# Kernel tuning notes

Measured on AMD Instinct MI355X. Metric: run time of the kernel, lower is better.

Reference implementation:

```python
import jax, jax.numpy as jnp
import numpy as np

B, S, D = 4, 2048, 128

def _phi(x, W, d):
    # original: phi(x) = (1/sqrt(M)) * exp(-0.5*||x||_2) * exp(W @ x), M = d
    proj = jnp.exp(jnp.einsum('...d,md->...m', x, W))          # [..., d]
    scale = jnp.exp(-0.5 * jnp.linalg.norm(x, axis=-1, keepdims=True))
    return (scale / jnp.sqrt(jnp.asarray(d, x.dtype))) * proj

def setup_inputs() -> dict:
    key = jax.random.key(0)
    k1, k2, k3, k4 = jax.random.split(key, 4)
    # scale 0.1 keeps exp(W @ x) well within fp32 range
    K = jax.random.normal(k1, (B, S, D), dtype=jnp.float32) * 0.1
    Q = jax.random.normal(k2, (B, S, D), dtype=jnp.float32) * 0.1
    V = jax.random.normal(k3, (B, S, D), dtype=jnp.float32) * 0.1
    W_phi = jax.random.normal(k4, (D, D), dtype=jnp.float32)
    sent_embed_slice = jnp.zeros((B, 1), dtype=jnp.float32)
    return {"K": K, "Q": Q, "V": V, "sent_embed_slice": sent_embed_slice,
            "max_seq_length": S, "qkv_size": D, "W_phi": W_phi}

def reference(K, Q, V, sent_embed_slice, max_seq_length, qkv_size, W_phi):
    d = qkv_size
    phiK = _phi(K, W_phi, d)   # [B, S, d]
    phiQ = _phi(Q, W_phi, d)   # [B, S, d]
    Bn = K.shape[0]

    def step(carry, inp):
        Mst, Nst = carry                       # [B, d, d], [B, d]
        pk, v, pq = inp                        # each [B, d]
        Mst = Mst + pk[:, :, None] * v[:, None, :]   # cumulative outer product
        Nst = Nst + pk                               # cumulative feature sum
        num = jnp.einsum('bd,bde->be', pq, Mst)      # phi(q) @ M
        r = jnp.einsum('bd,bd->b', pq, Nst)          # phi(q) . N
        out = num / (r + jnp.sign(r) * 1e-6)[:, None]
        return (Mst, Nst), out

    init = (jnp.zeros((Bn, d, d), K.dtype), jnp.zeros((Bn, d), K.dtype))
    xs = (jnp.swapaxes(phiK, 0, 1), jnp.swapaxes(V, 0, 1), jnp.swapaxes(phiQ, 0, 1))
    _, outs = jax.lax.scan(step, init, xs)    # outs: [S, B, d]
    return jnp.swapaxes(outs, 0, 1)           # [B, S, d]
```

## Files before the change

kernel.cpp:

```cpp
#include <hip/hip_runtime.h>

typedef float v4 __attribute__((ext_vector_type(4)));
typedef short s8v __attribute__((ext_vector_type(8)));
typedef float f4v __attribute__((ext_vector_type(4)));
typedef unsigned short u16;
typedef u16 us4 __attribute__((ext_vector_type(4)));
typedef u16 us8 __attribute__((ext_vector_type(8)));

#define OFF_PHIKB 0
#define OFF_PHIQB 524288
#define OFF_KVTB  1048576
#define OFF_PMB   3145728
#define OFF_N32   5242880
#define OFF_PN    5275648

__device__ inline u16 f2bf(float f) {
  union { float f; unsigned u; } v; v.f = f;
  unsigned r = v.u + 0x7fffu + ((v.u >> 16) & 1u);
  return (u16)(r >> 16);
}
__device__ inline float bf2f(u16 h) {
  union { unsigned u; float f; } v; v.u = ((unsigned)h) << 16; return v.f;
}

__global__ __launch_bounds__(256) void phikv_kernel(
    const float* __restrict__ K, const float* __restrict__ Q,
    const float* __restrict__ V, const float* __restrict__ W,
    u16* __restrict__ phiKb, u16* __restrict__ phiQb,
    u16* __restrict__ KVTb, float* __restrict__ N32) {
  __shared__ __align__(16) u16 smem[27136];
  __shared__ float srowsq[64];
  __shared__ float scl[64];
  u16* Xb = smem;
  u16* Wb = smem + 8704;
  u16* Pb = smem;
  u16* KdT = smem + 8704;
  u16* Vt = smem + 17920;

  const int tid = threadIdx.x;
  const bool isK = (blockIdx.y == 0);
  const float* X = isK ? K : Q;
  u16* outPhi = isK ? phiKb : phiQb;
  const int row0 = blockIdx.x * 64;
  const int wv = tid >> 6;
  const int lane = tid & 63;
  const int q = lane >> 4;
  const int ln = lane & 15;

#pragma unroll
  for (int k = 0; k < 8; k++) {
    int j = tid + k * 256;
    int r = j >> 5;
    int c4 = (j & 31) * 4;
    v4 x = *(const v4*)&X[(size_t)(row0 + r) * 128 + c4];
    us4 xb;
    float p = 0.f;
#pragma unroll
    for (int i = 0; i < 4; i++) { xb[i] = f2bf(x[i]); p += x[i] * x[i]; }
    *(us4*)&Xb[r * 136 + c4] = xb;
    p += __shfl_down(p, 16, 32);
    p += __shfl_down(p, 8, 32);
    p += __shfl_down(p, 4, 32);
    p += __shfl_down(p, 2, 32);
    p += __shfl_down(p, 1, 32);
    if ((tid & 31) == 0) srowsq[r] = p;
  }
#pragma unroll
  for (int k = 0; k < 16; k++) {
    int j = tid + k * 256;
    int r = j >> 5;
    int c4 = (j & 31) * 4;
    v4 w = *(const v4*)&W[(size_t)r * 128 + c4];
    us4 wb;
#pragma unroll
    for (int i = 0; i < 4; i++) wb[i] = f2bf(w[i]);
    *(us4*)&Wb[r * 136 + c4] = wb;
  }
  __syncthreads();
  if (tid < 64)
    scl[tid] = 0.08838834764831845f * __expf(-0.5f * sqrtf(srowsq[tid]));

  f4v acc[8];
#pragma unroll
  for (int ct = 0; ct < 8; ct++) acc[ct] = (f4v){0.f, 0.f, 0.f, 0.f};
#pragma unroll
  for (int ks = 0; ks < 4; ks++) {
    s8v a = *(const s8v*)&Xb[(wv * 16 + ln) * 136 + ks * 32 + q * 8];
#pragma unroll
    for (int ct = 0; ct < 8; ct++) {
      s8v bb = *(const s8v*)&Wb[(ct * 16 + ln) * 136 + ks * 32 + q * 8];
      acc[ct] = __builtin_amdgcn_mfma_f32_16x16x32_bf16(a, bb, acc[ct], 0, 0, 0);
    }
  }
  __syncthreads();

#pragma unroll
  for (int ct = 0; ct < 8; ct++) {
    us4 col;
#pragma unroll
    for (int r = 0; r < 4; r++) {
      int row = wv * 16 + q * 4 + r;
      u16 hv = f2bf(scl[row] * __expf(acc[ct][r]));
      Pb[row * 136 + ct * 16 + ln] = hv;
      col[r] = hv;
    }
    if (isK) *(us4*)&KdT[(ct * 16 + ln) * 72 + wv * 16 + q * 4] = col;
  }
  if (isK) {
#pragma unroll
    for (int k = 0; k < 8; k++) {
      int j = tid + k * 256;
      int s = j >> 5;
      int e4 = (j & 31) * 4;
      v4 vv = *(const v4*)&V[(size_t)(row0 + s) * 128 + e4];
#pragma unroll
      for (int i = 0; i < 4; i++) Vt[(e4 + i) * 72 + s] = f2bf(vv[i]);
    }
  }
  __syncthreads();

#pragma unroll
  for (int k = 0; k < 4; k++) {
    int j = tid + k * 256;
    int r = j >> 4;
    int d8 = (j & 15) * 8;
    *(us8*)&outPhi[(size_t)(row0 + r) * 128 + d8] = *(const us8*)&Pb[r * 136 + d8];
  }
  if (!isK) return;

  const int b = row0 >> 11;
  const int cgB = (row0 >> 5) & 63;

  {
    int c = tid >> 7;
    int d = tid & 127;
    float ns = 0.f;
#pragma unroll
    for (int s = 0; s < 32; s++) ns += bf2f(KdT[d * 72 + c * 32 + s]);
    N32[(size_t)(b * 64 + cgB + c) * 128 + d] = ns;
  }

#pragma unroll
  for (int c = 0; c < 2; c++) {
#pragma unroll
    for (int ei = 0; ei < 2; ei++) {
      const int et = wv * 2 + ei;
      s8v a = *(const s8v*)&Vt[(et * 16 + ln) * 72 + c * 32 + q * 8];
      f4v ac[8];
#pragma unroll
      for (int dt = 0; dt < 8; dt++) ac[dt] = (f4v){0.f, 0.f, 0.f, 0.f};
#pragma unroll
      for (int dt = 0; dt < 8; dt++) {
        s8v bb = *(const s8v*)&KdT[(dt * 16 + ln) * 72 + c * 32 + q * 8];
        ac[dt] = __builtin_amdgcn_mfma_f32_16x16x32_bf16(a, bb, ac[dt], 0, 0, 0);
      }
#pragma unroll
      for (int dt = 0; dt < 8; dt++)
#pragma unroll
        for (int r = 0; r < 4; r++) {
          int e = et * 16 + q * 4 + r;
          int d = dt * 16 + ln;
          KVTb[((size_t)(b * 128 + e) * 64 + (cgB + c)) * 128 + d] =
              f2bf(ac[dt][r]);
        }
    }
  }
}

__global__ __launch_bounds__(128) void prefix_kernel(
    const u16* __restrict__ KVTb, const float* __restrict__ N32,
    u16* __restrict__ PMb, float* __restrict__ PN) {
  const int tid = threadIdx.x;
  const int bid = blockIdx.x;
  if (bid < 512) {
    const size_t base = (size_t)bid * 64 * 128;
    float acc = 0.f;
#pragma unroll 8
    for (int c = 0; c < 64; c++) {
      PMb[base + c * 128 + tid] = f2bf(acc);
      acc += bf2f(KVTb[base + c * 128 + tid]);
    }
  } else {
    const int b = bid - 512;
    float acc = 0.f;
#pragma unroll 8
    for (int c = 0; c < 64; c++) {
      PN[(size_t)(b * 64 + c) * 128 + tid] = acc;
      acc += N32[(size_t)(b * 64 + c) * 128 + tid];
    }
  }
}

__global__ __launch_bounds__(256) void out_kernel(
    const u16* __restrict__ phiKb, const u16* __restrict__ phiQb,
    const float* __restrict__ V, const u16* __restrict__ PMb,
    const float* __restrict__ PN, float* __restrict__ out) {
  __shared__ __align__(16) u16 Qs[32][136];
  __shared__ __align__(16) u16 Ms[128][136];
  __shared__ __align__(16) u16 KsVt[128 * 40];
  __shared__ __align__(16) u16 Ps[32][40];
  __shared__ float Ns[128];
  __shared__ float rs[32];

  const int tid = threadIdx.x;
  const int b = blockIdx.x >> 6;
  const int c = blockIdx.x & 63;
  const int srow0 = b * 2048 + c * 32;
  const int wave = tid >> 6;
  const int lane = tid & 63;
  const int q = lane >> 4;
  const int ln = lane & 15;

#pragma unroll
  for (int k = 0; k < 2; k++) {
    int j = tid + k * 256;
    int t = j >> 4;
    int d8 = (j & 15) * 8;
    *(us8*)&Qs[t][d8] = *(const us8*)&phiQb[(size_t)(srow0 + t) * 128 + d8];
    *(us8*)&KsVt[t * 136 + d8] =
        *(const us8*)&phiKb[(size_t)(srow0 + t) * 128 + d8];
  }
#pragma unroll
  for (int k = 0; k < 8; k++) {
    int j = tid + k * 256;
    int e = j >> 4;
    int d8 = (j & 15) * 8;
    *(us8*)&Ms[e][d8] =
        *(const us8*)&PMb[((size_t)(b * 128 + e) * 64 + c) * 128 + d8];
  }
  if (tid < 128) Ns[tid] = PN[(size_t)(b * 64 + c) * 128 + tid];
  __syncthreads();

  {
    const int tr = wave >> 1, tc = wave & 1;
    f4v acc = {0.f, 0.f, 0.f, 0.f};
#pragma unroll
    for (int ks = 0; ks < 4; ks++) {
      s8v a = *(const s8v*)&Qs[tr * 16 + ln][ks * 32 + q * 8];
      s8v bb = *(const s8v*)&KsVt[(tc * 16 + ln) * 136 + ks * 32 + q * 8];
      acc = __builtin_amdgcn_mfma_f32_16x16x32_bf16(a, bb, acc, 0, 0, 0);
    }
    const int s_g = tc * 16 + ln;
#pragma unroll
    for (int r = 0; r < 4; r++) {
      int t_g = tr * 16 + q * 4 + r;
      Ps[t_g][s_g] = f2bf(s_g <= t_g ? acc[r] : 0.f);
    }
  }
  __syncthreads();

#pragma unroll
  for (int k = 0; k < 4; k++) {
    int j = tid + k * 256;
    int s = j & 31;
    int e4 = (j >> 5) * 4;
    v4 vv = *(const v4*)&V[(size_t)(srow0 + s) * 128 + e4];
#pragma unroll
    for (int i = 0; i < 4; i++) KsVt[(e4 + i) * 40 + s] = f2bf(vv[i]);
  }
  {
    const int t = tid >> 3;
    const int p8 = tid & 7;
    float rsl = 0.f;
#pragma unroll
    for (int s = p8; s < 32; s += 8) rsl += bf2f(Ps[t][s]);
#pragma unroll
    for (int d = p8; d < 128; d += 8) rsl += bf2f(Qs[t][d]) * Ns[d];
    rsl += __shfl_down(rsl, 4, 8);
    rsl += __shfl_down(rsl, 2, 8);
    rsl += __shfl_down(rsl, 1, 8);
    if (p8 == 0) rs[t] = rsl;
  }
  __syncthreads();

  const int e0 = wave * 32;
  f4v acc2[2][2];
#pragma unroll
  for (int i = 0; i < 2; i++)
#pragma unroll
    for (int j = 0; j < 2; j++) acc2[i][j] = (f4v){0.f, 0.f, 0.f, 0.f};

#pragma unroll
  for (int tr2 = 0; tr2 < 2; tr2++) {
    s8v a_p = *(const s8v*)&Ps[tr2 * 16 + ln][q * 8];
#pragma unroll
    for (int tc2 = 0; tc2 < 2; tc2++) {
      s8v b_v = *(const s8v*)&KsVt[(e0 + tc2 * 16 + ln) * 40 + q * 8];
      acc2[tr2][tc2] =
          __builtin_amdgcn_mfma_f32_16x16x32_bf16(a_p, b_v, acc2[tr2][tc2], 0, 0, 0);
    }
  }
#pragma unroll
  for (int ks = 0; ks < 4; ks++) {
#pragma unroll
    for (int tr2 = 0; tr2 < 2; tr2++) {
      s8v a_q = *(const s8v*)&Qs[tr2 * 16 + ln][ks * 32 + q * 8];
#pragma unroll
      for (int tc2 = 0; tc2 < 2; tc2++) {
        s8v b_m = *(const s8v*)&Ms[e0 + tc2 * 16 + ln][ks * 32 + q * 8];
        acc2[tr2][tc2] =
            __builtin_amdgcn_mfma_f32_16x16x32_bf16(a_q, b_m, acc2[tr2][tc2], 0, 0, 0);
      }
    }
  }

#pragma unroll
  for (int tr2 = 0; tr2 < 2; tr2++) {
#pragma unroll
    for (int r = 0; r < 4; r++) {
      int t_g = tr2 * 16 + q * 4 + r;
      float rv = rs[t_g];
      float den = rv + (rv > 0.f ? 1e-6f : (rv < 0.f ? -1e-6f : 0.f));
      float inv = 1.f / den;
#pragma unroll
      for (int tc2 = 0; tc2 < 2; tc2++) {
        int e_g = e0 + tc2 * 16 + ln;
        out[(size_t)(srow0 + t_g) * 128 + e_g] = acc2[tr2][tc2][r] * inv;
      }
    }
  }
}

extern "C" void kernel_launch(void* const* d_in, const int* in_sizes, int n_in,
                              void* d_out, int out_size, void* d_ws,
                              size_t ws_size, hipStream_t stream) {
  (void)in_sizes; (void)n_in; (void)out_size; (void)ws_size;
  const float* K = (const float*)d_in[0];
  const float* Q = (const float*)d_in[1];
  const float* V = (const float*)d_in[2];
  const float* W = (const float*)d_in[6];
  float* out = (float*)d_out;
  float* ws = (float*)d_ws;

  u16* phiKb = (u16*)(ws + OFF_PHIKB);
  u16* phiQb = (u16*)(ws + OFF_PHIQB);
  u16* KVTb = (u16*)(ws + OFF_KVTB);
  u16* PMb = (u16*)(ws + OFF_PMB);
  float* N32 = ws + OFF_N32;
  float* PN = ws + OFF_PN;

  phikv_kernel<<<dim3(128, 2), 256, 0, stream>>>(K, Q, V, W, phiKb, phiQb,
                                                 KVTb, N32);
  prefix_kernel<<<516, 128, 0, stream>>>(KVTb, N32, PMb, PN);
  out_kernel<<<256, 256, 0, stream>>>(phiKb, phiQb, V, PMb, PN, out);
}
```

Measured before the change: 95.58 us.

## Fuse three kernels into one persistent kernel with grid-wide barriers

Merges the phi/KV, prefix-scan and output kernels into a single 256-block launch separated by atomic-counter grid barriers, and adds a memset to reset the counters before launch. This removes two kernel launch gaps. The prefix scan now runs on only 33 blocks using 8-wide vector loads, and V loads are issued early into registers to overlap with other work. The risks are that the scan is concentrated on few blocks while the rest wait at the barrier, and that the barrier relies on all 256 blocks being resident at once.

```diff
diff --git a/kernel.cpp b/kernel.cpp
--- a/kernel.cpp
+++ b/kernel.cpp
@@ -1,6 +1,7 @@
 #include <hip/hip_runtime.h>
 
 typedef float v4 __attribute__((ext_vector_type(4)));
+typedef float v2 __attribute__((ext_vector_type(2)));
 typedef short s8v __attribute__((ext_vector_type(8)));
 typedef float f4v __attribute__((ext_vector_type(4)));
 typedef unsigned short u16;
@@ -13,6 +14,7 @@
 #define OFF_PMB   3145728
 #define OFF_N32   5242880
 #define OFF_PN    5275648
+#define OFF_BAR   5308416
 
 __device__ inline u16 f2bf(float f) {
   union { float f; unsigned u; } v; v.f = f;
@@ -23,299 +25,341 @@
   union { unsigned u; float f; } v; v.u = ((unsigned)h) << 16; return v.f;
 }
 
-__global__ __launch_bounds__(256) void phikv_kernel(
+__device__ inline void grid_barrier(unsigned* ctr, unsigned target) {
+  __syncthreads();
+  if (threadIdx.x == 0) {
+    __threadfence();
+    __hip_atomic_fetch_add(ctr, 1u, __ATOMIC_RELEASE, __HIP_MEMORY_SCOPE_AGENT);
+    while (__hip_atomic_load(ctr, __ATOMIC_ACQUIRE, __HIP_MEMORY_SCOPE_AGENT) <
+           target) {
+      __builtin_amdgcn_s_sleep(8);
+    }
+    __threadfence();
+  }
+  __syncthreads();
+}
+
+__global__ __launch_bounds__(256) void fused_kernel(
     const float* __restrict__ K, const float* __restrict__ Q,
     const float* __restrict__ V, const float* __restrict__ W,
-    u16* __restrict__ phiKb, u16* __restrict__ phiQb,
-    u16* __restrict__ KVTb, float* __restrict__ N32) {
-  __shared__ __align__(16) u16 smem[27136];
-  __shared__ float srowsq[64];
-  __shared__ float scl[64];
-  u16* Xb = smem;
-  u16* Wb = smem + 8704;
-  u16* Pb = smem;
-  u16* KdT = smem + 8704;
-  u16* Vt = smem + 17920;
+    u16* __restrict__ phiKb, u16* __restrict__ phiQb, u16* __restrict__ KVTb,
+    float* __restrict__ N32, u16* __restrict__ PMb, float* __restrict__ PN,
+    float* __restrict__ out, unsigned* __restrict__ bar) {
+  __shared__ __align__(16) u16 smem[28160];
+  __shared__ float sfl[160];
 
   const int tid = threadIdx.x;
-  const bool isK = (blockIdx.y == 0);
-  const float* X = isK ? K : Q;
-  u16* outPhi = isK ? phiKb : phiQb;
-  const int row0 = blockIdx.x * 64;
+  const int bid = blockIdx.x;
   const int wv = tid >> 6;
   const int lane = tid & 63;
   const int q = lane >> 4;
   const int ln = lane & 15;
 
-#pragma unroll
-  for (int k = 0; k < 8; k++) {
-    int j = tid + k * 256;
-    int r = j >> 5;
-    int c4 = (j & 31) * 4;
-    v4 x = *(const v4*)&X[(size_t)(row0 + r) * 128 + c4];
-    us4 xb;
-    float p = 0.f;
-#pragma unroll
-    for (int i = 0; i < 4; i++) { xb[i] = f2bf(x[i]); p += x[i] * x[i]; }
-    *(us4*)&Xb[r * 136 + c4] = xb;
-    p += __shfl_down(p, 16, 32);
-    p += __shfl_down(p, 8, 32);
-    p += __shfl_down(p, 4, 32);
-    p += __shfl_down(p, 2, 32);
-    p += __shfl_down(p, 1, 32);
-    if ((tid & 31) == 0) srowsq[r] = p;
+  {
+    const bool isK = (bid & 1) == 0;
+    const int slab = bid >> 1;
+    const float* X = isK ? K : Q;
+    u16* outPhi = isK ? phiKb : phiQb;
+    const int row0 = slab * 64;
+    u16* Xb = smem;
+    u16* Wb = smem + 8704;
+    u16* Pb = smem;
+    u16* KdT = smem + 8704;
+    u16* Vt = smem + 17920;
+    float* srowsq = sfl;
+    float* scl = sfl + 64;
+
+    v4 vpre[8];
+    if (isK) {
+#pragma unroll
+      for (int k = 0; k < 8; k++) {
+        int j = tid + k * 256;
+        int s = j >> 5;
+        int e4 = (j & 31) * 4;
+        vpre[k] = *(const v4*)&V[(size_t)(row0 + s) * 128 + e4];
+      }
+    }
+
+#pragma unroll
+    for (int k = 0; k < 8; k++) {
+      int j = tid + k * 256;
+      int r = j >> 5;
+      int c4 = (j & 31) * 4;
+      v4 x = *(const v4*)&X[(size_t)(row0 + r) * 128 + c4];
+      us4 xb;
+      float p = 0.f;
+#pragma unroll
+      for (int i = 0; i < 4; i++) { xb[i] = f2bf(x[i]); p += x[i] * x[i]; }
+      *(us4*)&Xb[r * 136 + c4] = xb;
+      p += __shfl_down(p, 16, 32);
+      p += __shfl_down(p, 8, 32);
+      p += __shfl_down(p, 4, 32);
+      p += __shfl_down(p, 2, 32);
+      p += __shfl_down(p, 1, 32);
+      if ((tid & 31) == 0) srowsq[r] = p;
+    }
+#pragma unroll
+    for (int k = 0; k < 16; k++) {
+      int j = tid + k * 256;
+      int r = j >> 5;
+      int c4 = (j & 31) * 4;
+      v4 w = *(const v4*)&W[(size_t)r * 128 + c4];
+      us4 wb;
+#pragma unroll
+      for (int i = 0; i < 4; i++) wb[i] = f2bf(w[i]);
+      *(us4*)&Wb[r * 136 + c4] = wb;
+    }
+    __syncthreads();
+    if (tid < 64)
+      scl[tid] = 0.08838834764831845f * __expf(-0.5f * sqrtf(srowsq[tid]));
+
+    f4v acc[8];
+#pragma unroll
+    for (int ct = 0; ct < 8; ct++) acc[ct] = (f4v){0.f, 0.f, 0.f, 0.f};
+#pragma unroll
+    for (int ks = 0; ks < 4; ks++) {
+      s8v a = *(const s8v*)&Xb[(wv * 16 + ln) * 136 + ks * 32 + q * 8];
+#pragma unroll
+      for (int ct = 0; ct < 8; ct++) {
+        s8v bb = *(const s8v*)&Wb[(ct * 16 + ln) * 136 + ks * 32 + q * 8];
+        acc[ct] =
+            __builtin_amdgcn_mfma_f32_16x16x32_bf16(a, bb, acc[ct], 0, 0, 0);
+      }
+    }
+    __syncthreads();
+
+#pragma unroll
+    for (int ct = 0; ct < 8; ct++) {
+      us4 col;
+#pragma unroll
+      for (int r = 0; r < 4; r++) {
+        int row = wv * 16 + q * 4 + r;
+        u16 hv = f2bf(scl[row] * __expf(acc[ct][r]));
+        Pb[row * 136 + ct * 16 + ln] = hv;
+        col[r] = hv;
+      }
+      if (isK) *(us4*)&KdT[(ct * 16 + ln) * 72 + wv * 16 + q * 4] = col;
+    }
+    if (isK) {
+#pragma unroll
+      for (int k = 0; k < 8; k++) {
+        int j = tid + k * 256;
+        int s = j >> 5;
+        int e4 = (j & 31) * 4;
+#pragma unroll
+        for (int i = 0; i < 4; i++) Vt[(e4 + i) * 72 + s] = f2bf(vpre[k][i]);
+      }
+    }
+    __syncthreads();
+
+#pragma unroll
+    for (int k = 0; k < 4; k++) {
+      int j = tid + k * 256;
+      int r = j >> 4;
+      int d8 = (j & 15) * 8;
+      *(us8*)&outPhi[(size_t)(row0 + r) * 128 + d8] =
+          *(const us8*)&Pb[r * 136 + d8];
+    }
+    if (isK) {
+      const int b = row0 >> 11;
+      const int cgB = (row0 >> 5) & 63;
+      {
+        int c = tid >> 7;
+        int d = tid & 127;
+        float ns = 0.f;
+#pragma unroll
+        for (int s = 0; s < 32; s++) ns += bf2f(KdT[d * 72 + c * 32 + s]);
+        N32[(size_t)(b * 64 + cgB + c) * 128 + d] = ns;
+      }
+#pragma unroll
+      for (int c = 0; c < 2; c++) {
+#pragma unroll
+        for (int ei = 0; ei < 2; ei++) {
+          const int et = wv * 2 + ei;
+          s8v a = *(const s8v*)&Vt[(et * 16 + ln) * 72 + c * 32 + q * 8];
+          f4v ac[8];
+#pragma unroll
+          for (int dt = 0; dt < 8; dt++) ac[dt] = (f4v){0.f, 0.f, 0.f, 0.f};
+#pragma unroll
+          for (int dt = 0; dt < 8; dt++) {
+            s8v bb = *(const s8v*)&KdT[(dt * 16 + ln) * 72 + c * 32 + q * 8];
+            ac[dt] =
+                __builtin_amdgcn_mfma_f32_16x16x32_bf16(a, bb, ac[dt], 0, 0, 0);
+          }
+#pragma unroll
+          for (int dt = 0; dt < 8; dt++)
+#pragma unroll
+            for (int r = 0; r < 4; r++) {
+              int e = et * 16 + q * 4 + r;
+              int d = dt * 16 + ln;
+              KVTb[((size_t)(b * 128 + e) * 64 + (cgB + c)) * 128 + d] =
+                  f2bf(ac[dt][r]);
+            }
+        }
+      }
+    }
   }
-#pragma unroll
-  for (int k = 0; k < 16; k++) {
-    int j = tid + k * 256;
-    int r = j >> 5;
-    int c4 = (j & 31) * 4;
-    v4 w = *(const v4*)&W[(size_t)r * 128 + c4];
-    us4 wb;
-#pragma unroll
-    for (int i = 0; i < 4; i++) wb[i] = f2bf(w[i]);
-    *(us4*)&Wb[r * 136 + c4] = wb;
+  grid_barrier(bar + 0, 256);
+
+  if (bid < 32) {
+    const int r = bid * 16 + (tid >> 4);
+    const int d8 = (tid & 15) * 8;
+    const size_t base = (size_t)r * (64 * 128);
+    float acc[8];
+#pragma unroll
+    for (int i = 0; i < 8; i++) acc[i] = 0.f;
+#pragma unroll 4
+    for (int c = 0; c < 64; c++) {
+      us8 st;
+#pragma unroll
+      for (int i = 0; i < 8; i++) st[i] = f2bf(acc[i]);
+      *(us8*)&PMb[base + c * 128 + d8] = st;
+      us8 kv = *(const us8*)&KVTb[base + c * 128 + d8];
+#pragma unroll
+      for (int i = 0; i < 8; i++) acc[i] += bf2f(kv[i]);
+    }
+  } else if (bid == 32) {
+    const int b = tid >> 6;
+    const int d2 = (tid & 63) * 2;
+    float a0 = 0.f, a1 = 0.f;
+#pragma unroll 4
+    for (int c = 0; c < 64; c++) {
+      size_t idx = (size_t)(b * 64 + c) * 128 + d2;
+      *(v2*)&PN[idx] = (v2){a0, a1};
+      v2 nv = *(const v2*)&N32[idx];
+      a0 += nv[0];
+      a1 += nv[1];
+    }
   }
-  __syncthreads();
-  if (tid < 64)
-    scl[tid] = 0.08838834764831845f * __expf(-0.5f * sqrtf(srowsq[tid]));
-
-  f4v acc[8];
-#pragma unroll
-  for (int ct = 0; ct < 8; ct++) acc[ct] = (f4v){0.f, 0.f, 0.f, 0.f};
-#pragma unroll
-  for (int ks = 0; ks < 4; ks++) {
-    s8v a = *(const s8v*)&Xb[(wv * 16 + ln) * 136 + ks * 32 + q * 8];
-#pragma unroll
-    for (int ct = 0; ct < 8; ct++) {
-      s8v bb = *(const s8v*)&Wb[(ct * 16 + ln) * 136 + ks * 32 + q * 8];
-      acc[ct] = __builtin_amdgcn_mfma_f32_16x16x32_bf16(a, bb, acc[ct], 0, 0, 0);
-    }
-  }
-  __syncthreads();
-
-#pragma unroll
-  for (int ct = 0; ct < 8; ct++) {
-    us4 col;
-#pragma unroll
-    for (int r = 0; r < 4; r++) {
-      int row = wv * 16 + q * 4 + r;
-      u16 hv = f2bf(scl[row] * __expf(acc[ct][r]));
-      Pb[row * 136 + ct * 16 + ln] = hv;
-      col[r] = hv;
-    }
-    if (isK) *(us4*)&KdT[(ct * 16 + ln) * 72 + wv * 16 + q * 4] = col;
-  }
-  if (isK) {
+  grid_barrier(bar + 1, 256);
+
+  {
+    const int b = bid >> 6;
+    const int c = bid & 63;
+    const int srow0 = b * 2048 + c * 32;
+    u16* Qs = smem;
+    u16* Ms = smem + 4352;
+    u16* KsVt = smem + 21760;
+    u16* Ps = smem + 26880;
+    float* Ns = sfl;
+    float* rs = sfl + 128;
+
+    v4 vpre3[4];
+#pragma unroll
+    for (int k = 0; k < 4; k++) {
+      int j = tid + k * 256;
+      int s = j & 31;
+      int e4 = (j >> 5) * 4;
+      vpre3[k] = *(const v4*)&V[(size_t)(srow0 + s) * 128 + e4];
+    }
+
+#pragma unroll
+    for (int k = 0; k < 2; k++) {
+      int j = tid + k * 256;
+      int t = j >> 4;
+      int d8 = (j & 15) * 8;
+      *(us8*)&Qs[t * 136 + d8] =
+          *(const us8*)&phiQb[(size_t)(srow0 + t) * 128 + d8];
+      *(us8*)&KsVt[t * 136 + d8] =
+          *(const us8*)&phiKb[(size_t)(srow0 + t) * 128 + d8];
+    }
 #pragma unroll
     for (int k = 0; k < 8; k++) {
       int j = tid + k * 256;
-      int s = j >> 5;
-      int e4 = (j & 31) * 4;
-      v4 vv = *(const v4*)&V[(size_t)(row0 + s) * 128 + e4];
-#pragma unroll
-      for (int i = 0; i < 4; i++) Vt[(e4 + i) * 72 + s] = f2bf(vv[i]);
-    }
-  }
-  __syncthreads();
-
-#pragma unroll
-  for (int k = 0; k < 4; k++) {
-    int j = tid + k * 256;
-    int r = j >> 4;
-    int d8 = (j & 15) * 8;
-    *(us8*)&outPhi[(size_t)(row0 + r) * 128 + d8] = *(const us8*)&Pb[r * 136 + d8];
-  }
-  if (!isK) return;
-
-  const int b = row0 >> 11;
-  const int cgB = (row0 >> 5) & 63;
-
-  {
-    int c = tid >> 7;
-    int d = tid & 127;
-    float ns = 0.f;
-#pragma unroll
-    for (int s = 0; s < 32; s++) ns += bf2f(KdT[d * 72 + c * 32 + s]);
-    N32[(size_t)(b * 64 + cgB + c) * 128 + d] = ns;
-  }
-
-#pragma unroll
-  for (int c = 0; c < 2; c++) {
-#pragma unroll
-    for (int ei = 0; ei < 2; ei++) {
-      const int et = wv * 2 + ei;
-      s8v a = *(const s8v*)&Vt[(et * 16 + ln) * 72 + c * 32 + q * 8];
-      f4v ac[8];
-#pragma unroll
-      for (int dt = 0; dt < 8; dt++) ac[dt] = (f4v){0.f, 0.f, 0.f, 0.f};
-#pragma unroll
-      for (int dt = 0; dt < 8; dt++) {
-        s8v bb = *(const s8v*)&KdT[(dt * 16 + ln) * 72 + c * 32 + q * 8];
-        ac[dt] = __builtin_amdgcn_mfma_f32_16x16x32_bf16(a, bb, ac[dt], 0, 0, 0);
-      }
-#pragma unroll
-      for (int dt = 0; dt < 8; dt++)
-#pragma unroll
-        for (int r = 0; r < 4; r++) {
-          int e = et * 16 + q * 4 + r;
-          int d = dt * 16 + ln;
-          KVTb[((size_t)(b * 128 + e) * 64 + (cgB + c)) * 128 + d] =
-              f2bf(ac[dt][r]);
+      int e = j >> 4;
+      int d8 = (j & 15) * 8;
+      *(us8*)&Ms[e * 136 + d8] =
+          *(const us8*)&PMb[((size_t)(b * 128 + e) * 64 + c) * 128 + d8];
+    }
+    if (tid < 128) Ns[tid] = PN[(size_t)(b * 64 + c) * 128 + tid];
+    __syncthreads();
+
+    {
+      const int tr = wv >> 1, tc = wv & 1;
+      f4v acc = {0.f, 0.f, 0.f, 0.f};
+#pragma unroll
+      for (int ks = 0; ks < 4; ks++) {
+        s8v a = *(const s8v*)&Qs[(tr * 16 + ln) * 136 + ks * 32 + q * 8];
+        s8v bb = *(const s8v*)&KsVt[(tc * 16 + ln) * 136 + ks * 32 + q * 8];
+        acc = __builtin_amdgcn_mfma_f32_16x16x32_bf16(a, bb, acc, 0, 0, 0);
+      }
+      const int s_g = tc * 16 + ln;
+#pragma unroll
+      for (int r = 0; r < 4; r++) {
+        int t_g = tr * 16 + q * 4 + r;
+        Ps[t_g * 40 + s_g] = f2bf(s_g <= t_g ? acc[r] : 0.f);
+      }
+    }
+    __syncthreads();
+
+#pragma unroll
+    for (int k = 0; k < 4; k++) {
+      int j = tid + k * 256;
+      int s = j & 31;
+      int e4 = (j >> 5) * 4;
+#pragma unroll
+      for (int i = 0; i < 4; i++) KsVt[(e4 + i) * 40 + s] = f2bf(vpre3[k][i]);
+    }
+    {
+      const int t = tid >> 3;
+      const int p8 = tid & 7;
+      float rsl = 0.f;
+#pragma unroll
+      for (int s = p8; s < 32; s += 8) rsl += bf2f(Ps[t * 40 + s]);
+#pragma unroll
+      for (int d = p8; d < 128; d += 8) rsl += bf2f(Qs[t * 136 + d]) * Ns[d];
+      rsl += __shfl_down(rsl, 4, 8);
+      rsl += __shfl_down(rsl, 2, 8);
+      rsl += __shfl_down(rsl, 1, 8);
+      if (p8 == 0) rs[t] = rsl;
+    }
+    __syncthreads();
+
+    const int e0 = wv * 32;
+    f4v acc2[2][2];
+#pragma unroll
+    for (int i = 0; i < 2; i++)
+#pragma unroll
+      for (int j = 0; j < 2; j++) acc2[i][j] = (f4v){0.f, 0.f, 0.f, 0.f};
+
+#pragma unroll
+    for (int tr2 = 0; tr2 < 2; tr2++) {
+      s8v a_p = *(const s8v*)&Ps[(tr2 * 16 + ln) * 40 + q * 8];
+#pragma unroll
+      for (int tc2 = 0; tc2 < 2; tc2++) {
+        s8v b_v = *(const s8v*)&KsVt[(e0 + tc2 * 16 + ln) * 40 + q * 8];
+        acc2[tr2][tc2] = __builtin_amdgcn_mfma_f32_16x16x32_bf16(
+            a_p, b_v, acc2[tr2][tc2], 0, 0, 0);
+      }
+    }
+#pragma unroll
+    for (int ks = 0; ks < 4; ks++) {
+#pragma unroll
+      for (int tr2 = 0; tr2 < 2; tr2++) {
+        s8v a_q = *(const s8v*)&Qs[(tr2 * 16 + ln) * 136 + ks * 32 + q * 8];
+#pragma unroll
+        for (int tc2 = 0; tc2 < 2; tc2++) {
+          s8v b_m =
+              *(const s8v*)&Ms[(e0 + tc2 * 16 + ln) * 136 + ks * 32 + q * 8];
+          acc2[tr2][tc2] = __builtin_amdgcn_mfma_f32_16x16x32_bf16(
+              a_q, b_m, acc2[tr2][tc2], 0, 0, 0);
         }
-    }
-  }
-}
-
-__global__ __launch_bounds__(128) void prefix_kernel(
-    const u16* __restrict__ KVTb, const float* __restrict__ N32,
-    u16* __restrict__ PMb, float* __restrict__ PN) {
-  const int tid = threadIdx.x;
-  const int bid = blockIdx.x;
-  if (bid < 512) {
-    const size_t base = (size_t)bid * 64 * 128;
-    float acc = 0.f;
-#pragma unroll 8
-    for (int c = 0; c < 64; c++) {
-      PMb[base + c * 128 + tid] = f2bf(acc);
-      acc += bf2f(KVTb[base + c * 128 + tid]);
-    }
-  } else {
-    const int b = bid - 512;
-    float acc = 0.f;
-#pragma unroll 8
-    for (int c = 0; c < 64; c++) {
-      PN[(size_t)(b * 64 + c) * 128 + tid] = acc;
-      acc += N32[(size_t)(b * 64 + c) * 128 + tid];
-    }
-  }
-}
-
-__global__ __launch_bounds__(256) void out_kernel(
-    const u16* __restrict__ phiKb, const u16* __restrict__ phiQb,
-    const float* __restrict__ V, const u16* __restrict__ PMb,
-    const float* __restrict__ PN, float* __restrict__ out) {
-  __shared__ __align__(16) u16 Qs[32][136];
-  __shared__ __align__(16) u16 Ms[128][136];
-  __shared__ __align__(16) u16 KsVt[128 * 40];
-  __shared__ __align__(16) u16 Ps[32][40];
-  __shared__ float Ns[128];
-  __shared__ float rs[32];
-
-  const int tid = threadIdx.x;
-  const int b = blockIdx.x >> 6;
-  const int c = blockIdx.x & 63;
-  const int srow0 = b * 2048 + c * 32;
-  const int wave = tid >> 6;
-  const int lane = tid & 63;
-  const int q = lane >> 4;
-  const int ln = lane & 15;
-
-#pragma unroll
-  for (int k = 0; k < 2; k++) {
-    int j = tid + k * 256;
-    int t = j >> 4;
-    int d8 = (j & 15) * 8;
-    *(us8*)&Qs[t][d8] = *(const us8*)&phiQb[(size_t)(srow0 + t) * 128 + d8];
-    *(us8*)&KsVt[t * 136 + d8] =
-        *(const us8*)&phiKb[(size_t)(srow0 + t) * 128 + d8];
-  }
-#pragma unroll
-  for (int k = 0; k < 8; k++) {
-    int j = tid + k * 256;
-    int e = j >> 4;
-    int d8 = (j & 15) * 8;
-    *(us8*)&Ms[e][d8] =
-        *(const us8*)&PMb[((size_t)(b * 128 + e) * 64 + c) * 128 + d8];
-  }
-  if (tid < 128) Ns[tid] = PN[(size_t)(b * 64 + c) * 128 + tid];
-  __syncthreads();
-
-  {
-    const int tr = wave >> 1, tc = wave & 1;
-    f4v acc = {0.f, 0.f, 0.f, 0.f};
-#pragma unroll
-    for (int ks = 0; ks < 4; ks++) {
-      s8v a = *(const s8v*)&Qs[tr * 16 + ln][ks * 32 + q * 8];
-      s8v bb = *(const s8v*)&KsVt[(tc * 16 + ln) * 136 + ks * 32 + q * 8];
-      acc = __builtin_amdgcn_mfma_f32_16x16x32_bf16(a, bb, acc, 0, 0, 0);
-    }
-    const int s_g = tc * 16 + ln;
-#pragma unroll
-    for (int r = 0; r < 4; r++) {
-      int t_g = tr * 16 + q * 4 + r;
-      Ps[t_g][s_g] = f2bf(s_g <= t_g ? acc[r] : 0.f);
-    }
-  }
-  __syncthreads();
-
-#pragma unroll
-  for (int k = 0; k < 4; k++) {
-    int j = tid + k * 256;
-    int s = j & 31;
-    int e4 = (j >> 5) * 4;
-    v4 vv = *(const v4*)&V[(size_t)(srow0 + s) * 128 + e4];
-#pragma unroll
-    for (int i = 0; i < 4; i++) KsVt[(e4 + i) * 40 + s] = f2bf(vv[i]);
-  }
-  {
-    const int t = tid >> 3;
-    const int p8 = tid & 7;
-    float rsl = 0.f;
-#pragma unroll
-    for (int s = p8; s < 32; s += 8) rsl += bf2f(Ps[t][s]);
-#pragma unroll
-    for (int d = p8; d < 128; d += 8) rsl += bf2f(Qs[t][d]) * Ns[d];
-    rsl += __shfl_down(rsl, 4, 8);
-    rsl += __shfl_down(rsl, 2, 8);
-    rsl += __shfl_down(rsl, 1, 8);
-    if (p8 == 0) rs[t] = rsl;
-  }
-  __syncthreads();
-
-  const int e0 = wave * 32;
-  f4v acc2[2][2];
-#pragma unroll
-  for (int i = 0; i < 2; i++)
-#pragma unroll
-    for (int j = 0; j < 2; j++) acc2[i][j] = (f4v){0.f, 0.f, 0.f, 0.f};
-
-#pragma unroll
-  for (int tr2 = 0; tr2 < 2; tr2++) {
-    s8v a_p = *(const s8v*)&Ps[tr2 * 16 + ln][q * 8];
-#pragma unroll
-    for (int tc2 = 0; tc2 < 2; tc2++) {
-      s8v b_v = *(const s8v*)&KsVt[(e0 + tc2 * 16 + ln) * 40 + q * 8];
-      acc2[tr2][tc2] =
-          __builtin_amdgcn_mfma_f32_16x16x32_bf16(a_p, b_v, acc2[tr2][tc2], 0, 0, 0);
-    }
-  }
-#pragma unroll
-  for (int ks = 0; ks < 4; ks++) {
+      }
+    }
+
 #pragma unroll
     for (int tr2 = 0; tr2 < 2; tr2++) {
-      s8v a_q = *(const s8v*)&Qs[tr2 * 16 + ln][ks * 32 + q * 8];
-#pragma unroll
-      for (int tc2 = 0; tc2 < 2; tc2++) {
-        s8v b_m = *(const s8v*)&Ms[e0 + tc2 * 16 + ln][ks * 32 + q * 8];
-        acc2[tr2][tc2] =
-            __builtin_amdgcn_mfma_f32_16x16x32_bf16(a_q, b_m, acc2[tr2][tc2], 0, 0, 0);
-      }
-    }
-  }
-
-#pragma unroll
-  for (int tr2 = 0; tr2 < 2; tr2++) {
-#pragma unroll
-    for (int r = 0; r < 4; r++) {
-      int t_g = tr2 * 16 + q * 4 + r;
-      float rv = rs[t_g];
-      float den = rv + (rv > 0.f ? 1e-6f : (rv < 0.f ? -1e-6f : 0.f));
-      float inv = 1.f / den;
-#pragma unroll
-      for (int tc2 = 0; tc2 < 2; tc2++) {
-        int e_g = e0 + tc2 * 16 + ln;
-        out[(size_t)(srow0 + t_g) * 128 + e_g] = acc2[tr2][tc2][r] * inv;
+#pragma unroll
+      for (int r = 0; r < 4; r++) {
+        int t_g = tr2 * 16 + q * 4 + r;
+        float rv = rs[t_g];
+        float den = rv + (rv > 0.f ? 1e-6f : (rv < 0.f ? -1e-6f : 0.f));
+        float inv = 1.f / den;
+#pragma unroll
+        for (int tc2 = 0; tc2 < 2; tc2++) {
+          int e_g = e0 + tc2 * 16 + ln;
+          out[(size_t)(srow0 + t_g) * 128 + e_g] = acc2[tr2][tc2][r] * inv;
+        }
       }
     }
   }
@@ -338,9 +382,9 @@
   u16* PMb = (u16*)(ws + OFF_PMB);
   float* N32 = ws + OFF_N32;
   float* PN = ws + OFF_PN;
-
-  phikv_kernel<<<dim3(128, 2), 256, 0, stream>>>(K, Q, V, W, phiKb, phiQb,
-                                                 KVTb, N32);
-  prefix_kernel<<<516, 128, 0, stream>>>(KVTb, N32, PMb, PN);
-  out_kernel<<<256, 256, 0, stream>>>(phiKb, phiQb, V, PMb, PN, out);
-}
+  unsigned* bar = (unsigned*)(ws + OFF_BAR);
+
+  hipMemsetAsync(bar, 0, 2 * sizeof(unsigned), stream);
+  fused_kernel<<<256, 256, 0, stream>>>(K, Q, V, W, phiKb, phiQb, KVTb, N32,
+                                        PMb, PN, out, bar);
+}
```

Measured after the change: 180.6 us. 89.0% more time.

## Double chunk size to 64, split output by column quarters, vectorize prefix scan

Applied to the files above, without the earlier changes.

The sequence chunk size goes from 32 to 64. This halves the per-chunk KV state written to and read from the workspace, and halves the number of sequential prefix steps. phikv_kernel now runs 512 threads and issues its V loads early so they overlap the feature computation. The prefix kernel moves to 65 blocks with vectorized bf16 and float2 accesses. out_kernel splits each 64-row chunk into four 32-column slices, giving 512 blocks, and skips the masked upper-triangle MFMA tiles. The cost is that each slice block reloads the phiQ and phiK tiles and recomputes the intra-chunk score matrix and row sums.

```diff
diff --git a/kernel.cpp b/kernel.cpp
--- a/kernel.cpp
+++ b/kernel.cpp
@@ -1,18 +1,20 @@
 #include <hip/hip_runtime.h>
 
 typedef float v4 __attribute__((ext_vector_type(4)));
+typedef float v2 __attribute__((ext_vector_type(2)));
 typedef short s8v __attribute__((ext_vector_type(8)));
 typedef float f4v __attribute__((ext_vector_type(4)));
 typedef unsigned short u16;
+typedef u16 us2 __attribute__((ext_vector_type(2)));
 typedef u16 us4 __attribute__((ext_vector_type(4)));
 typedef u16 us8 __attribute__((ext_vector_type(8)));
 
 #define OFF_PHIKB 0
 #define OFF_PHIQB 524288
 #define OFF_KVTB  1048576
-#define OFF_PMB   3145728
-#define OFF_N32   5242880
-#define OFF_PN    5275648
+#define OFF_PMB   2097152
+#define OFF_N32   3145728
+#define OFF_PN    3162112
 
 __device__ inline u16 f2bf(float f) {
   union { float f; unsigned u; } v; v.f = f;
@@ -23,7 +25,7 @@
   union { unsigned u; float f; } v; v.u = ((unsigned)h) << 16; return v.f;
 }
 
-__global__ __launch_bounds__(256) void phikv_kernel(
+__global__ __launch_bounds__(512) void phikv_kernel(
     const float* __restrict__ K, const float* __restrict__ Q,
     const float* __restrict__ V, const float* __restrict__ W,
     u16* __restrict__ phiKb, u16* __restrict__ phiQb,
@@ -47,9 +49,21 @@
   const int q = lane >> 4;
   const int ln = lane & 15;
 
-#pragma unroll
-  for (int k = 0; k < 8; k++) {
-    int j = tid + k * 256;
+  v4 vpa[2], vpb[2];
+  if (isK) {
+#pragma unroll
+    for (int k = 0; k < 2; k++) {
+      int j = tid + k * 512;
+      int s0 = (j & 31) * 2;
+      int e4 = (j >> 5) * 4;
+      vpa[k] = *(const v4*)&V[(size_t)(row0 + s0) * 128 + e4];
+      vpb[k] = *(const v4*)&V[(size_t)(row0 + s0 + 1) * 128 + e4];
+    }
+  }
+
+#pragma unroll
+  for (int k = 0; k < 4; k++) {
+    int j = tid + k * 512;
     int r = j >> 5;
     int c4 = (j & 31) * 4;
     v4 x = *(const v4*)&X[(size_t)(row0 + r) * 128 + c4];
@@ -66,8 +80,8 @@
     if ((tid & 31) == 0) srowsq[r] = p;
   }
 #pragma unroll
-  for (int k = 0; k < 16; k++) {
-    int j = tid + k * 256;
+  for (int k = 0; k < 8; k++) {
+    int j = tid + k * 512;
     int r = j >> 5;
     int c4 = (j & 31) * 4;
     v4 w = *(const v4*)&W[(size_t)r * 128 + c4];
@@ -80,48 +94,53 @@
   if (tid < 64)
     scl[tid] = 0.08838834764831845f * __expf(-0.5f * sqrtf(srowsq[tid]));
 
-  f4v acc[8];
-#pragma unroll
-  for (int ct = 0; ct < 8; ct++) acc[ct] = (f4v){0.f, 0.f, 0.f, 0.f};
+  const int tr = wv >> 1;
+  const int cb = (wv & 1) * 4;
+  f4v acc[4];
+#pragma unroll
+  for (int i = 0; i < 4; i++) acc[i] = (f4v){0.f, 0.f, 0.f, 0.f};
 #pragma unroll
   for (int ks = 0; ks < 4; ks++) {
-    s8v a = *(const s8v*)&Xb[(wv * 16 + ln) * 136 + ks * 32 + q * 8];
-#pragma unroll
-    for (int ct = 0; ct < 8; ct++) {
-      s8v bb = *(const s8v*)&Wb[(ct * 16 + ln) * 136 + ks * 32 + q * 8];
-      acc[ct] = __builtin_amdgcn_mfma_f32_16x16x32_bf16(a, bb, acc[ct], 0, 0, 0);
-    }
-  }
-  __syncthreads();
-
-#pragma unroll
-  for (int ct = 0; ct < 8; ct++) {
+    s8v a = *(const s8v*)&Xb[(tr * 16 + ln) * 136 + ks * 32 + q * 8];
+#pragma unroll
+    for (int i = 0; i < 4; i++) {
+      s8v bb = *(const s8v*)&Wb[((cb + i) * 16 + ln) * 136 + ks * 32 + q * 8];
+      acc[i] = __builtin_amdgcn_mfma_f32_16x16x32_bf16(a, bb, acc[i], 0, 0, 0);
+    }
+  }
+  __syncthreads();
+
+#pragma unroll
+  for (int i = 0; i < 4; i++) {
+    const int ct = cb + i;
     us4 col;
 #pragma unroll
     for (int r = 0; r < 4; r++) {
-      int row = wv * 16 + q * 4 + r;
-      u16 hv = f2bf(scl[row] * __expf(acc[ct][r]));
+      int row = tr * 16 + q * 4 + r;
+      u16 hv = f2bf(scl[row] * __expf(acc[i][r]));
       Pb[row * 136 + ct * 16 + ln] = hv;
       col[r] = hv;
     }
-    if (isK) *(us4*)&KdT[(ct * 16 + ln) * 72 + wv * 16 + q * 4] = col;
+    if (isK) *(us4*)&KdT[(ct * 16 + ln) * 72 + tr * 16 + q * 4] = col;
   }
   if (isK) {
 #pragma unroll
-    for (int k = 0; k < 8; k++) {
-      int j = tid + k * 256;
-      int s = j >> 5;
-      int e4 = (j & 31) * 4;
-      v4 vv = *(const v4*)&V[(size_t)(row0 + s) * 128 + e4];
-#pragma unroll
-      for (int i = 0; i < 4; i++) Vt[(e4 + i) * 72 + s] = f2bf(vv[i]);
-    }
-  }
-  __syncthreads();
-
-#pragma unroll
-  for (int k = 0; k < 4; k++) {
-    int j = tid + k * 256;
+    for (int k = 0; k < 2; k++) {
+      int j = tid + k * 512;
+      int s0 = (j & 31) * 2;
+      int e4 = (j >> 5) * 4;
+#pragma unroll
+      for (int i = 0; i < 4; i++) {
+        us2 w2 = {f2bf(vpa[k][i]), f2bf(vpb[k][i])};
+        *(us2*)&Vt[(e4 + i) * 72 + s0] = w2;
+      }
+    }
+  }
+  __syncthreads();
+
+#pragma unroll
+  for (int k = 0; k < 2; k++) {
+    int j = tid + k * 512;
     int r = j >> 4;
     int d8 = (j & 15) * 8;
     *(us8*)&outPhi[(size_t)(row0 + r) * 128 + d8] = *(const us8*)&Pb[r * 136 + d8];
@@ -129,64 +148,71 @@
   if (!isK) return;
 
   const int b = row0 >> 11;
-  const int cgB = (row0 >> 5) & 63;
+  const int c = (row0 >> 6) & 31;
+
+  if (tid < 128) {
+    float ns = 0.f;
+#pragma unroll
+    for (int s = 0; s < 64; s++) ns += bf2f(KdT[tid * 72 + s]);
+    N32[(size_t)(b * 32 + c) * 128 + tid] = ns;
+  }
 
   {
-    int c = tid >> 7;
-    int d = tid & 127;
-    float ns = 0.f;
-#pragma unroll
-    for (int s = 0; s < 32; s++) ns += bf2f(KdT[d * 72 + c * 32 + s]);
-    N32[(size_t)(b * 64 + cgB + c) * 128 + d] = ns;
-  }
-
-#pragma unroll
-  for (int c = 0; c < 2; c++) {
-#pragma unroll
-    for (int ei = 0; ei < 2; ei++) {
-      const int et = wv * 2 + ei;
-      s8v a = *(const s8v*)&Vt[(et * 16 + ln) * 72 + c * 32 + q * 8];
-      f4v ac[8];
-#pragma unroll
-      for (int dt = 0; dt < 8; dt++) ac[dt] = (f4v){0.f, 0.f, 0.f, 0.f};
-#pragma unroll
-      for (int dt = 0; dt < 8; dt++) {
-        s8v bb = *(const s8v*)&KdT[(dt * 16 + ln) * 72 + c * 32 + q * 8];
-        ac[dt] = __builtin_amdgcn_mfma_f32_16x16x32_bf16(a, bb, ac[dt], 0, 0, 0);
+    const int et = wv;
+    s8v a0 = *(const s8v*)&Vt[(et * 16 + ln) * 72 + q * 8];
+    s8v a1 = *(const s8v*)&Vt[(et * 16 + ln) * 72 + 32 + q * 8];
+    f4v ac[8];
+#pragma unroll
+    for (int dt = 0; dt < 8; dt++) ac[dt] = (f4v){0.f, 0.f, 0.f, 0.f};
+#pragma unroll
+    for (int dt = 0; dt < 8; dt++) {
+      s8v b0 = *(const s8v*)&KdT[(dt * 16 + ln) * 72 + q * 8];
+      ac[dt] = __builtin_amdgcn_mfma_f32_16x16x32_bf16(a0, b0, ac[dt], 0, 0, 0);
+      s8v b1 = *(const s8v*)&KdT[(dt * 16 + ln) * 72 + 32 + q * 8];
+      ac[dt] = __builtin_amdgcn_mfma_f32_16x16x32_bf16(a1, b1, ac[dt], 0, 0, 0);
+    }
+#pragma unroll
+    for (int dt = 0; dt < 8; dt++)
+#pragma unroll
+      for (int r = 0; r < 4; r++) {
+        int e = et * 16 + q * 4 + r;
+        int d = dt * 16 + ln;
+        KVTb[((size_t)(b * 128 + e) * 32 + c) * 128 + d] = f2bf(ac[dt][r]);
       }
-#pragma unroll
-      for (int dt = 0; dt < 8; dt++)
-#pragma unroll
-        for (int r = 0; r < 4; r++) {
-          int e = et * 16 + q * 4 + r;
-          int d = dt * 16 + ln;
-          KVTb[((size_t)(b * 128 + e) * 64 + (cgB + c)) * 128 + d] =
-              f2bf(ac[dt][r]);
-        }
-    }
-  }
-}
-
-__global__ __launch_bounds__(128) void prefix_kernel(
+  }
+}
+
+__global__ __launch_bounds__(256) void prefix_kernel(
     const u16* __restrict__ KVTb, const float* __restrict__ N32,
     u16* __restrict__ PMb, float* __restrict__ PN) {
   const int tid = threadIdx.x;
   const int bid = blockIdx.x;
-  if (bid < 512) {
-    const size_t base = (size_t)bid * 64 * 128;
-    float acc = 0.f;
-#pragma unroll 8
-    for (int c = 0; c < 64; c++) {
-      PMb[base + c * 128 + tid] = f2bf(acc);
-      acc += bf2f(KVTb[base + c * 128 + tid]);
+  if (bid < 64) {
+    const int r = bid * 8 + (tid >> 5);
+    const int d4 = (tid & 31) * 4;
+    const size_t base = (size_t)r * (32 * 128);
+    float acc[4] = {0.f, 0.f, 0.f, 0.f};
+#pragma unroll 4
+    for (int c = 0; c < 32; c++) {
+      us4 st;
+#pragma unroll
+      for (int i = 0; i < 4; i++) st[i] = f2bf(acc[i]);
+      *(us4*)&PMb[base + c * 128 + d4] = st;
+      us4 kv = *(const us4*)&KVTb[base + c * 128 + d4];
+#pragma unroll
+      for (int i = 0; i < 4; i++) acc[i] += bf2f(kv[i]);
     }
   } else {
-    const int b = bid - 512;
-    float acc = 0.f;
-#pragma unroll 8
-    for (int c = 0; c < 64; c++) {
-      PN[(size_t)(b * 64 + c) * 128 + tid] = acc;
-      acc += N32[(size_t)(b * 64 + c) * 128 + tid];
+    const int b = tid >> 6;
+    const int d2 = (tid & 63) * 2;
+    float a0 = 0.f, a1 = 0.f;
+#pragma unroll 4
+    for (int c = 0; c < 32; c++) {
+      size_t idx = (size_t)(b * 32 + c) * 128 + d2;
+      *(v2*)&PN[idx] = (v2){a0, a1};
+      v2 nv = *(const v2*)&N32[idx];
+      a0 += nv[0];
+      a1 += nv[1];
     }
   }
 }
@@ -195,128 +221,122 @@
     const u16* __restrict__ phiKb, const u16* __restrict__ phiQb,
     const float* __restrict__ V, const u16* __restrict__ PMb,
     const float* __restrict__ PN, float* __restrict__ out) {
-  __shared__ __align__(16) u16 Qs[32][136];
-  __shared__ __align__(16) u16 Ms[128][136];
-  __shared__ __align__(16) u16 KsVt[128 * 40];
-  __shared__ __align__(16) u16 Ps[32][40];
+  __shared__ __align__(16) u16 Qs[64 * 136];
+  __shared__ __align__(16) u16 Ks[64 * 136];
+  __shared__ __align__(16) u16 Ms[32 * 136];
+  __shared__ __align__(16) u16 Vt[32 * 72];
+  __shared__ __align__(16) u16 Ps[64 * 72];
   __shared__ float Ns[128];
-  __shared__ float rs[32];
+  __shared__ float rs[64];
 
   const int tid = threadIdx.x;
-  const int b = blockIdx.x >> 6;
-  const int c = blockIdx.x & 63;
-  const int srow0 = b * 2048 + c * 32;
-  const int wave = tid >> 6;
+  const int id = blockIdx.x;
+  const int h = id & 3;
+  const int c = (id >> 2) & 31;
+  const int b = id >> 7;
+  const int srow0 = b * 2048 + c * 64;
+  const int ecol0 = h * 32;
+  const int wv = tid >> 6;
   const int lane = tid & 63;
   const int q = lane >> 4;
   const int ln = lane & 15;
 
-#pragma unroll
-  for (int k = 0; k < 2; k++) {
+  const int vs0 = (tid & 31) * 2;
+  const int ve4 = (tid >> 5) * 4;
+  v4 va = *(const v4*)&V[(size_t)(srow0 + vs0) * 128 + ecol0 + ve4];
+  v4 vb = *(const v4*)&V[(size_t)(srow0 + vs0 + 1) * 128 + ecol0 + ve4];
+
+#pragma unroll
+  for (int k = 0; k < 4; k++) {
     int j = tid + k * 256;
     int t = j >> 4;
     int d8 = (j & 15) * 8;
-    *(us8*)&Qs[t][d8] = *(const us8*)&phiQb[(size_t)(srow0 + t) * 128 + d8];
-    *(us8*)&KsVt[t * 136 + d8] =
-        *(const us8*)&phiKb[(size_t)(srow0 + t) * 128 + d8];
-  }
-#pragma unroll
-  for (int k = 0; k < 8; k++) {
+    *(us8*)&Qs[t * 136 + d8] = *(const us8*)&phiQb[(size_t)(srow0 + t) * 128 + d8];
+    *(us8*)&Ks[t * 136 + d8] = *(const us8*)&phiKb[(size_t)(srow0 + t) * 128 + d8];
+  }
+#pragma unroll
+  for (int k = 0; k < 2; k++) {
     int j = tid + k * 256;
     int e = j >> 4;
     int d8 = (j & 15) * 8;
-    *(us8*)&Ms[e][d8] =
-        *(const us8*)&PMb[((size_t)(b * 128 + e) * 64 + c) * 128 + d8];
-  }
-  if (tid < 128) Ns[tid] = PN[(size_t)(b * 64 + c) * 128 + tid];
+    *(us8*)&Ms[e * 136 + d8] =
+        *(const us8*)&PMb[((size_t)(b * 128 + ecol0 + e) * 32 + c) * 128 + d8];
+  }
+  if (tid < 128) Ns[tid] = PN[(size_t)(b * 32 + c) * 128 + tid];
+#pragma unroll
+  for (int i = 0; i < 4; i++) {
+    us2 w2 = {f2bf(va[i]), f2bf(vb[i])};
+    *(us2*)&Vt[(ve4 + i) * 72 + vs0] = w2;
+  }
   __syncthreads();
 
   {
-    const int tr = wave >> 1, tc = wave & 1;
-    f4v acc = {0.f, 0.f, 0.f, 0.f};
+    const int tr = wv;
+    for (int tc = 0; tc < 4; tc++) {
+      f4v acc = {0.f, 0.f, 0.f, 0.f};
+      if (tc <= tr) {
+#pragma unroll
+        for (int ks = 0; ks < 4; ks++) {
+          s8v a = *(const s8v*)&Qs[(tr * 16 + ln) * 136 + ks * 32 + q * 8];
+          s8v bb = *(const s8v*)&Ks[(tc * 16 + ln) * 136 + ks * 32 + q * 8];
+          acc = __builtin_amdgcn_mfma_f32_16x16x32_bf16(a, bb, acc, 0, 0, 0);
+        }
+      }
+      const int s_g = tc * 16 + ln;
+#pragma unroll
+      for (int r = 0; r < 4; r++) {
+        int t_g = tr * 16 + q * 4 + r;
+        Ps[t_g * 72 + s_g] = f2bf(s_g <= t_g ? acc[r] : 0.f);
+      }
+    }
+  }
+  __syncthreads();
+
+  {
+    const int t = tid >> 2;
+    const int p4 = tid & 3;
+    float rsl = 0.f;
+#pragma unroll
+    for (int s = p4; s < 64; s += 4) rsl += bf2f(Ps[t * 72 + s]);
+#pragma unroll
+    for (int d = p4; d < 128; d += 4) rsl += bf2f(Qs[t * 136 + d]) * Ns[d];
+    rsl += __shfl_down(rsl, 2, 4);
+    rsl += __shfl_down(rsl, 1, 4);
+    if (p4 == 0) rs[t] = rsl;
+  }
+
+  const int et = wv & 1;
+  f4v acc2[2];
+#pragma unroll
+  for (int i = 0; i < 2; i++) acc2[i] = (f4v){0.f, 0.f, 0.f, 0.f};
+#pragma unroll
+  for (int i = 0; i < 2; i++) {
+    const int tr2 = (wv >> 1) + 2 * i;
+#pragma unroll
+    for (int ks2 = 0; ks2 < 2; ks2++) {
+      s8v a_p = *(const s8v*)&Ps[(tr2 * 16 + ln) * 72 + ks2 * 32 + q * 8];
+      s8v b_v = *(const s8v*)&Vt[(et * 16 + ln) * 72 + ks2 * 32 + q * 8];
+      acc2[i] = __builtin_amdgcn_mfma_f32_16x16x32_bf16(a_p, b_v, acc2[i], 0, 0, 0);
+    }
 #pragma unroll
     for (int ks = 0; ks < 4; ks++) {
-      s8v a = *(const s8v*)&Qs[tr * 16 + ln][ks * 32 + q * 8];
-      s8v bb = *(const s8v*)&KsVt[(tc * 16 + ln) * 136 + ks * 32 + q * 8];
-      acc = __builtin_amdgcn_mfma_f32_16x16x32_bf16(a, bb, acc, 0, 0, 0);
-    }
-    const int s_g = tc * 16 + ln;
-#pragma unroll
-    for (int r = 0; r < 4; r++) {
-      int t_g = tr * 16 + q * 4 + r;
-      Ps[t_g][s_g] = f2bf(s_g <= t_g ? acc[r] : 0.f);
-    }
-  }
-  __syncthreads();
-
-#pragma unroll
-  for (int k = 0; k < 4; k++) {
-    int j = tid + k * 256;
-    int s = j & 31;
-    int e4 = (j >> 5) * 4;
-    v4 vv = *(const v4*)&V[(size_t)(srow0 + s) * 128 + e4];
-#pragma unroll
-    for (int i = 0; i < 4; i++) KsVt[(e4 + i) * 40 + s] = f2bf(vv[i]);
-  }
-  {
-    const int t = tid >> 3;
-    const int p8 = tid & 7;
-    float rsl = 0.f;
-#pragma unroll
-    for (int s = p8; s < 32; s += 8) rsl += bf2f(Ps[t][s]);
-#pragma unroll
-    for (int d = p8; d < 128; d += 8) rsl += bf2f(Qs[t][d]) * Ns[d];
-    rsl += __shfl_down(rsl, 4, 8);
-    rsl += __shfl_down(rsl, 2, 8);
-    rsl += __shfl_down(rsl, 1, 8);
-    if (p8 == 0) rs[t] = rsl;
-  }
-  __syncthreads();
-
-  const int e0 = wave * 32;
-  f4v acc2[2][2];
-#pragma unroll
-  for (int i = 0; i < 2; i++)
-#pragma unroll
-    for (int j = 0; j < 2; j++) acc2[i][j] = (f4v){0.f, 0.f, 0.f, 0.f};
-
-#pragma unroll
-  for (int tr2 = 0; tr2 < 2; tr2++) {
-    s8v a_p = *(const s8v*)&Ps[tr2 * 16 + ln][q * 8];
-#pragma unroll
-    for (int tc2 = 0; tc2 < 2; tc2++) {
-      s8v b_v = *(const s8v*)&KsVt[(e0 + tc2 * 16 + ln) * 40 + q * 8];
-      acc2[tr2][tc2] =
-          __builtin_amdgcn_mfma_f32_16x16x32_bf16(a_p, b_v, acc2[tr2][tc2], 0, 0, 0);
-    }
-  }
-#pragma unroll
-  for (int ks = 0; ks < 4; ks++) {
-#pragma unroll
-    for (int tr2 = 0; tr2 < 2; tr2++) {
-      s8v a_q = *(const s8v*)&Qs[tr2 * 16 + ln][ks * 32 + q * 8];
-#pragma unroll
-      for (int tc2 = 0; tc2 < 2; tc2++) {
-        s8v b_m = *(const s8v*)&Ms[e0 + tc2 * 16 + ln][ks * 32 + q * 8];
-        acc2[tr2][tc2] =
-            __builtin_amdgcn_mfma_f32_16x16x32_bf16(a_q, b_m, acc2[tr2][tc2], 0, 0, 0);
-      }
-    }
-  }
-
-#pragma unroll
-  for (int tr2 = 0; tr2 < 2; tr2++) {
+      s8v a_q = *(const s8v*)&Qs[(tr2 * 16 + ln) * 136 + ks * 32 + q * 8];
+      s8v b_m = *(const s8v*)&Ms[(et * 16 + ln) * 136 + ks * 32 + q * 8];
+      acc2[i] = __builtin_amdgcn_mfma_f32_16x16x32_bf16(a_q, b_m, acc2[i], 0, 0, 0);
+    }
+  }
+  __syncthreads();
+
+#pragma unroll
+  for (int i = 0; i < 2; i++) {
+    const int tr2 = (wv >> 1) + 2 * i;
 #pragma unroll
     for (int r = 0; r < 4; r++) {
       int t_g = tr2 * 16 + q * 4 + r;
       float rv = rs[t_g];
       float den = rv + (rv > 0.f ? 1e-6f : (rv < 0.f ? -1e-6f : 0.f));
-      float inv = 1.f / den;
-#pragma unroll
-      for (int tc2 = 0; tc2 < 2; tc2++) {
-        int e_g = e0 + tc2 * 16 + ln;
-        out[(size_t)(srow0 + t_g) * 128 + e_g] = acc2[tr2][tc2][r] * inv;
-      }
+      out[(size_t)(srow0 + t_g) * 128 + ecol0 + et * 16 + ln] =
+          acc2[i][r] / den;
     }
   }
 }
@@ -339,8 +359,8 @@
   float* N32 = ws + OFF_N32;
   float* PN = ws + OFF_PN;
 
-  phikv_kernel<<<dim3(128, 2), 256, 0, stream>>>(K, Q, V, W, phiKb, phiQb,
+  phikv_kernel<<<dim3(128, 2), 512, 0, stream>>>(K, Q, V, W, phiKb, phiQb,
                                                  KVTb, N32);
-  prefix_kernel<<<516, 128, 0, stream>>>(KVTb, N32, PMb, PN);
-  out_kernel<<<256, 256, 0, stream>>>(phiKb, phiQb, V, PMb, PN, out);
-}
+  prefix_kernel<<<65, 256, 0, stream>>>(KVTb, N32, PMb, PN);
+  out_kernel<<<512, 256, 0, stream>>>(phiKb, phiQb, V, PMb, PN, out);
+}
```

After: 94.00 us. Within noise of the previous version (-1.6%).
